# Kernel optimization log

Hardware: AMD Instinct MI355X
Metric: run time of the kernel (lower is better)

## Reference

```python
import jax, jax.numpy as jnp
import numpy as np

NUM_HEADS = 12

def setup_inputs() -> dict:
    key = jax.random.key(0)
    k1, k2, k3 = jax.random.split(key, 3)
    B, H, W, C = 8, 32, 32, 768
    x = jax.random.normal(k1, (B, H, W, C), dtype=jnp.float32)
    qkv_w = jax.random.normal(k2, (3 * C, C), dtype=jnp.float32) * (C ** -0.5)
    qkv_b = jnp.zeros((3 * C,), dtype=jnp.float32)
    proj_w = jax.random.normal(k3, (C, C), dtype=jnp.float32) * (C ** -0.5)
    proj_b = jnp.zeros((C,), dtype=jnp.float32)
    return {"x": x, "qkv_w": qkv_w, "qkv_b": qkv_b, "proj_w": proj_w, "proj_b": proj_b}

def reference(x, qkv_w, qkv_b, proj_w, proj_b):
    B, H, W, C = x.shape
    N = H * W
    h = NUM_HEADS
    d = C // h
    scale = d ** -0.5
    xf = x.reshape(B, N, C)
    # fused QKV projection: [B,N,3C] -> [3,B,h,N,d]
    qkv = (xf @ qkv_w.T + qkv_b).reshape(B, N, 3, h, d).transpose(2, 0, 3, 1, 4)
    q, k, v = qkv[0], qkv[1], qkv[2]  # rope = Identity
    # scaled dot-product attention
    scores = jnp.einsum('bhnd,bhmd->bhnm', q, k) * scale
    attn = jax.nn.softmax(scores, axis=-1)
    out = jnp.einsum('bhnm,bhmd->bhnd', attn, v)
    out = out.transpose(0, 2, 1, 3).reshape(B, N, C)
    out = out @ proj_w.T + proj_b
    return out.reshape(B, H, W, C)
```

## Files before the change

### kernel.cpp

```cpp
#include <hip/hip_runtime.h>
#include <math.h>

#define AS1 __attribute__((address_space(1)))
#define AS3 __attribute__((address_space(3)))

typedef __attribute__((ext_vector_type(8))) short bf16x8;
typedef __attribute__((ext_vector_type(4))) float f32x4;

__device__ __forceinline__ unsigned short f2bf(float f) {
    union { float f; unsigned int i; } v; v.f = f;
    unsigned int r = v.i + 0x7FFFu + ((v.i >> 16) & 1u);
    return (unsigned short)(r >> 16);
}

__device__ __forceinline__ void store_out(float* p, float v) { *p = v; }
__device__ __forceinline__ void store_out(unsigned short* p, float v) { *p = f2bf(v); }

#define N1C (8192 * 768 / 4)
#define N2C (2304 * 768 / 4)
#define N3C (768 * 768 / 4)

__global__ void cvt_all(const float* __restrict__ x, const float* __restrict__ w1,
                        const float* __restrict__ w2,
                        unsigned short* __restrict__ xb, unsigned short* __restrict__ w1b,
                        unsigned short* __restrict__ w2b)
{
    int i = blockIdx.x * blockDim.x + threadIdx.x;
    const float4* s; ushort4* d; int k;
    if (i < N1C)            { s = (const float4*)x;  d = (ushort4*)xb;  k = i; }
    else if (i < N1C + N2C) { s = (const float4*)w1; d = (ushort4*)w1b; k = i - N1C; }
    else if (i < N1C + N2C + N3C) { s = (const float4*)w2; d = (ushort4*)w2b; k = i - N1C - N2C; }
    else return;
    const float4 v = s[k];
    ushort4 o;
    o.x = f2bf(v.x); o.y = f2bf(v.y); o.z = f2bf(v.z); o.w = f2bf(v.w);
    d[k] = o;
}

template <typename OutT>
__global__ __launch_bounds__(256, 2)
void gemm_bt_128(const unsigned short* __restrict__ A,
                 const unsigned short* __restrict__ W,
                 const float* __restrict__ bias,
                 OutT* __restrict__ Cmat,
                 int M, int N, int K)
{
    __shared__ __align__(16) unsigned short As[128 * 32];
    __shared__ __align__(16) unsigned short Bs[128 * 32];

    const int tid  = threadIdx.x;
    const int wave = tid >> 6;
    const int lane = tid & 63;
    const int quad = lane >> 4;
    const int l15  = lane & 15;
    const int wr   = wave >> 1;
    const int wc   = wave & 1;

    const int m0 = blockIdx.x * 128;
    const int n0 = blockIdx.y * 128;

    const int srow = wave * 32 + (lane >> 2);
    const int scol = (lane & 3) * 8;

    const unsigned short* Ag0 = A + (size_t)(m0 + srow) * K + scol;
    const unsigned short* Ag1 = A + (size_t)(m0 + srow + 16) * K + scol;
    const unsigned short* Wg0 = W + (size_t)(n0 + srow) * K + scol;
    const unsigned short* Wg1 = W + (size_t)(n0 + srow + 16) * K + scol;

    unsigned short* As0 = As + (wave * 2 + 0) * 512 + lane * 8;
    unsigned short* As1 = As + (wave * 2 + 1) * 512 + lane * 8;
    unsigned short* Bs0 = Bs + (wave * 2 + 0) * 512 + lane * 8;
    unsigned short* Bs1 = Bs + (wave * 2 + 1) * 512 + lane * 8;

    f32x4 acc[4][4];
#pragma unroll
    for (int i = 0; i < 4; ++i)
#pragma unroll
        for (int j = 0; j < 4; ++j) acc[i][j] = (f32x4){0.f, 0.f, 0.f, 0.f};

    for (int k0 = 0; k0 < K; k0 += 32) {
        __syncthreads();
        __builtin_amdgcn_global_load_lds((AS1 void*)(Ag0 + k0), (AS3 void*)As0, 16, 0, 0);
        __builtin_amdgcn_global_load_lds((AS1 void*)(Ag1 + k0), (AS3 void*)As1, 16, 0, 0);
        __builtin_amdgcn_global_load_lds((AS1 void*)(Wg0 + k0), (AS3 void*)Bs0, 16, 0, 0);
        __builtin_amdgcn_global_load_lds((AS1 void*)(Wg1 + k0), (AS3 void*)Bs1, 16, 0, 0);
        __syncthreads();

        bf16x8 af[4], bfr[4];
#pragma unroll
        for (int i = 0; i < 4; ++i)
            af[i] = *(const bf16x8*)(As + (wr * 64 + i * 16 + l15) * 32 + quad * 8);
#pragma unroll
        for (int j = 0; j < 4; ++j)
            bfr[j] = *(const bf16x8*)(Bs + (wc * 64 + j * 16 + l15) * 32 + quad * 8);
#pragma unroll
        for (int i = 0; i < 4; ++i)
#pragma unroll
            for (int j = 0; j < 4; ++j)
                acc[i][j] = __builtin_amdgcn_mfma_f32_16x16x32_bf16(af[i], bfr[j], acc[i][j], 0, 0, 0);
    }

#pragma unroll
    for (int i = 0; i < 4; ++i) {
        const int row = m0 + wr * 64 + i * 16 + quad * 4;
#pragma unroll
        for (int j = 0; j < 4; ++j) {
            const int col = n0 + wc * 64 + j * 16 + l15;
            const float bv = bias[col];
#pragma unroll
            for (int r = 0; r < 4; ++r)
                store_out(&Cmat[(size_t)(row + r) * N + col], acc[i][j][r] + bv);
        }
    }
}

#define NTOK 1024
#define CCH  768
#define HD   64

__global__ __launch_bounds__(256)
void pack_vT(const unsigned short* __restrict__ qkv, unsigned short* __restrict__ vT)
{
    __shared__ __align__(16) unsigned short Ls[64 * 72];
    const int tile = blockIdx.x;
    const int bh   = blockIdx.y;
    const int b = bh / 12, h = bh % 12;
    const int t = threadIdx.x;

    const int tok = t >> 2, c = (t & 3) * 16;
    const unsigned short* src = qkv + (size_t)(b * NTOK + tile * 64 + tok) * (3 * CCH)
                                    + 2 * CCH + h * HD + c;
    bf16x8 a0 = *(const bf16x8*)src;
    bf16x8 a1 = *(const bf16x8*)(src + 8);
    *(bf16x8*)&Ls[tok * 72 + c]     = a0;
    *(bf16x8*)&Ls[tok * 72 + c + 8] = a1;
    __syncthreads();

    const int r = t >> 5;
    const int dbase = (r >> 1) * 16;
    const int k5b   = (r & 1) * 32;
    unsigned short outv[16];
#pragma unroll
    for (int u = 0; u < 2; ++u) {
        const int L  = (t & 31) * 2 + u;
        const int d  = dbase + (L & 15);
        const int k0 = k5b + (L >> 4) * 8;
#pragma unroll
        for (int j = 0; j < 8; ++j) outv[u * 8 + j] = Ls[(k0 + j) * 72 + d];
    }
    unsigned short* dst = vT + ((size_t)(bh * 16 + tile) * 8 + r) * 512 + (t & 31) * 16;
    *(bf16x8*)dst       = *(bf16x8*)&outv[0];
    *(bf16x8*)(dst + 8) = *(bf16x8*)&outv[8];
}

__global__ __launch_bounds__(256, 3)
void attn_fused(const unsigned short* __restrict__ qkv,
                const unsigned short* __restrict__ vT,
                unsigned short* __restrict__ aout)
{
    __shared__ __align__(16) unsigned short Kf[2][8 * 512];
    __shared__ __align__(16) unsigned short Vt[2][8 * 512];
    __shared__ __align__(16) unsigned short Ps[16 * 512];

    const int tid  = threadIdx.x;
    const int wave = tid >> 6;
    const int lane = tid & 63;
    const int quad = lane >> 4;
    const int l15  = lane & 15;

    const int lin = blockIdx.x;
    const int bh  = lin % 96;
    const int qt  = lin / 96;
    const int b   = bh / 12;
    const int h   = bh % 12;

    const size_t rs = 3 * CCH;
    const unsigned short* Qg = qkv + (size_t)b * NTOK * rs + (size_t)h * HD;
    const unsigned short* Kg = Qg + CCH;
    const unsigned short* vTb = vT + (size_t)bh * 16 * 8 * 512;

    const int q0 = qt * 128;

    bf16x8 qf[2][2];
#pragma unroll
    for (int qb = 0; qb < 2; ++qb)
#pragma unroll
        for (int ks = 0; ks < 2; ++ks)
            qf[qb][ks] = *(const bf16x8*)(Qg + (size_t)(q0 + wave * 32 + qb * 16 + l15) * rs
                                              + ks * 32 + quad * 8);

    f32x4 oacc[2][4];
#pragma unroll
    for (int qb = 0; qb < 2; ++qb)
#pragma unroll
        for (int nb = 0; nb < 4; ++nb) oacc[qb][nb] = (f32x4){0.f, 0.f, 0.f, 0.f};
    float lrow[2] = {0.f, 0.f};

    const unsigned short* kdma = Kg + (size_t)(wave * 16 + l15) * rs + quad * 8;

#pragma unroll
    for (int ks = 0; ks < 2; ++ks)
        __builtin_amdgcn_global_load_lds((AS1 void*)(kdma + ks * 32),
            (AS3 void*)(Kf[0] + (wave * 2 + ks) * 512 + lane * 8), 16, 0, 0);
#pragma unroll
    for (int u = 0; u < 2; ++u)
        __builtin_amdgcn_global_load_lds((AS1 void*)(vTb + (size_t)(wave * 2 + u) * 512 + lane * 8),
            (AS3 void*)(Vt[0] + (wave * 2 + u) * 512 + lane * 8), 16, 0, 0);

    for (int t = 0; t < 16; ++t) {
        const int cur = t & 1;
        __syncthreads();

        if (t < 15) {
            const int nxt = cur ^ 1;
#pragma unroll
            for (int ks = 0; ks < 2; ++ks)
                __builtin_amdgcn_global_load_lds((AS1 void*)(kdma + (size_t)((t + 1) * 64) * rs + ks * 32),
                    (AS3 void*)(Kf[nxt] + (wave * 2 + ks) * 512 + lane * 8), 16, 0, 0);
#pragma unroll
            for (int u = 0; u < 2; ++u)
                __builtin_amdgcn_global_load_lds((AS1 void*)(vTb + ((size_t)(t + 1) * 8 + wave * 2 + u) * 512 + lane * 8),
                    (AS3 void*)(Vt[nxt] + (wave * 2 + u) * 512 + lane * 8), 16, 0, 0);
        }

        f32x4 sacc[2][4];
#pragma unroll
        for (int qb = 0; qb < 2; ++qb)
#pragma unroll
            for (int jk = 0; jk < 4; ++jk) sacc[qb][jk] = (f32x4){0.f, 0.f, 0.f, 0.f};
#pragma unroll
        for (int ks = 0; ks < 2; ++ks) {
            bf16x8 kf[4];
#pragma unroll
            for (int jk = 0; jk < 4; ++jk)
                kf[jk] = *(const bf16x8*)(Kf[cur] + (jk * 2 + ks) * 512 + lane * 8);
#pragma unroll
            for (int qb = 0; qb < 2; ++qb)
#pragma unroll
                for (int jk = 0; jk < 4; ++jk)
                    sacc[qb][jk] = __builtin_amdgcn_mfma_f32_16x16x32_bf16(
                        kf[jk], qf[qb][ks], sacc[qb][jk], 0, 0, 0);
        }

#pragma unroll
        for (int qb = 0; qb < 2; ++qb) {
            float rsum = 0.f;
#pragma unroll
            for (int jk = 0; jk < 4; ++jk)
#pragma unroll
                for (int r = 0; r < 4; ++r) {
                    const float p = __expf(sacc[qb][jk][r] * 0.125f);
                    sacc[qb][jk][r] = p;
                    rsum += p;
                }
            rsum += __shfl_xor(rsum, 16);
            rsum += __shfl_xor(rsum, 32);
            lrow[qb] += rsum;

#pragma unroll
            for (int jk = 0; jk < 4; ++jk) {
                ushort4 pk;
                pk.x = f2bf(sacc[qb][jk][0]);
                pk.y = f2bf(sacc[qb][jk][1]);
                pk.z = f2bf(sacc[qb][jk][2]);
                pk.w = f2bf(sacc[qb][jk][3]);
                const int region = (wave * 2 + qb) * 2 + (jk >> 1);
                const int quadR  = (jk & 1) * 2 + (quad >> 1);
                const int off    = region * 512 + (quadR * 16 + l15) * 8 + (quad & 1) * 4;
                *(ushort4*)&Ps[off] = pk;
            }
        }

#pragma unroll
        for (int ks2 = 0; ks2 < 2; ++ks2) {
            bf16x8 pf[2], vf[4];
#pragma unroll
            for (int qb = 0; qb < 2; ++qb)
                pf[qb] = *(const bf16x8*)(Ps + ((wave * 2 + qb) * 2 + ks2) * 512 + lane * 8);
#pragma unroll
            for (int nb = 0; nb < 4; ++nb)
                vf[nb] = *(const bf16x8*)(Vt[cur] + (nb * 2 + ks2) * 512 + lane * 8);
#pragma unroll
            for (int qb = 0; qb < 2; ++qb)
#pragma unroll
                for (int nb = 0; nb < 4; ++nb)
                    oacc[qb][nb] = __builtin_amdgcn_mfma_f32_16x16x32_bf16(
                        vf[nb], pf[qb], oacc[qb][nb], 0, 0, 0);
        }
    }

#pragma unroll
    for (int qb = 0; qb < 2; ++qb) {
        const float inv = 1.f / lrow[qb];
        const size_t tok = (size_t)(b * NTOK + q0 + wave * 32 + qb * 16 + l15);
#pragma unroll
        for (int nb = 0; nb < 4; ++nb) {
            ushort4 o;
            o.x = f2bf(oacc[qb][nb][0] * inv);
            o.y = f2bf(oacc[qb][nb][1] * inv);
            o.z = f2bf(oacc[qb][nb][2] * inv);
            o.w = f2bf(oacc[qb][nb][3] * inv);
            *(ushort4*)(aout + tok * CCH + h * HD + nb * 16 + quad * 4) = o;
        }
    }
}

extern "C" void kernel_launch(void* const* d_in, const int* in_sizes, int n_in,
                              void* d_out, int out_size, void* d_ws, size_t ws_size,
                              hipStream_t stream)
{
    const float* x      = (const float*)d_in[0];
    const float* qkv_w  = (const float*)d_in[1];
    const float* qkv_b  = (const float*)d_in[2];
    const float* proj_w = (const float*)d_in[3];
    const float* proj_b = (const float*)d_in[4];
    float* out = (float*)d_out;

    unsigned short* qkv = (unsigned short*)d_ws;
    unsigned short* att = qkv + (size_t)8192 * 2304;
    unsigned short* xb  = att + (size_t)8192 * 768;
    unsigned short* wqb = xb  + (size_t)8192 * 768;
    unsigned short* wpb = wqb + (size_t)2304 * 768;
    unsigned short* vT  = xb;

    dim3 blk(256);
    cvt_all<<<dim3((N1C + N2C + N3C + 255) / 256), blk, 0, stream>>>(x, qkv_w, proj_w, xb, wqb, wpb);
    gemm_bt_128<unsigned short><<<dim3(64, 18), blk, 0, stream>>>(xb, wqb, qkv_b, qkv, 8192, 2304, 768);
    pack_vT<<<dim3(16, 96), blk, 0, stream>>>(qkv, vT);
    attn_fused<<<dim3(768), blk, 0, stream>>>(qkv, vT, att);
    gemm_bt_128<float><<<dim3(64, 6), blk, 0, stream>>>(att, wpb, proj_b, out, 8192, 768, 768);
}
```

Before: 207.0 us.

## Fuse V transpose into QKV GEMM epilogue and fold softmax scale into Q

The QKV GEMM now gets its own kernel whose epilogue writes Q and K into a narrower 1536-wide buffer, with Q pre-scaled by 1/sqrt(d), and writes V directly in the transposed tiled layout the attention kernel expects. This removes the separate pack_vT kernel and its extra read and write of V. The attention kernel halves its P staging buffer by interleaving P stores with PV MFMAs per k-half, raises launch bounds occupancy to 4, and uses a cheaper perm-based bf16 packing. The new packing rounds with a plain +0x8000 instead of round-to-nearest-even, which slightly changes numerics.

Result: faster. 187.0 us (-9.7%).

```diff
diff --git a/kernel.cpp b/kernel.cpp
--- a/kernel.cpp
+++ b/kernel.cpp
@@ -13,8 +13,18 @@
     return (unsigned short)(r >> 16);
 }
 
+__device__ __forceinline__ unsigned int pack2bf(float lo, float hi) {
+    union { float f; unsigned int i; } a, b; a.f = lo; b.f = hi;
+    return __builtin_amdgcn_perm(b.i + 0x8000u, a.i + 0x8000u, 0x07060302u);
+}
+
 __device__ __forceinline__ void store_out(float* p, float v) { *p = v; }
 __device__ __forceinline__ void store_out(unsigned short* p, float v) { *p = f2bf(v); }
+
+#define NTOK 1024
+#define CCH  768
+#define HD   64
+#define QKS  1536
 
 #define N1C (8192 * 768 / 4)
 #define N2C (2304 * 768 / 4)
@@ -114,53 +124,118 @@
     }
 }
 
-#define NTOK 1024
-#define CCH  768
-#define HD   64
-
-__global__ __launch_bounds__(256)
-void pack_vT(const unsigned short* __restrict__ qkv, unsigned short* __restrict__ vT)
+__global__ __launch_bounds__(256, 2)
+void gemm_qkv(const unsigned short* __restrict__ A,
+              const unsigned short* __restrict__ W,
+              const float* __restrict__ bias,
+              unsigned short* __restrict__ qk,
+              unsigned short* __restrict__ vT)
 {
-    __shared__ __align__(16) unsigned short Ls[64 * 72];
-    const int tile = blockIdx.x;
-    const int bh   = blockIdx.y;
-    const int b = bh / 12, h = bh % 12;
-    const int t = threadIdx.x;
-
-    const int tok = t >> 2, c = (t & 3) * 16;
-    const unsigned short* src = qkv + (size_t)(b * NTOK + tile * 64 + tok) * (3 * CCH)
-                                    + 2 * CCH + h * HD + c;
-    bf16x8 a0 = *(const bf16x8*)src;
-    bf16x8 a1 = *(const bf16x8*)(src + 8);
-    *(bf16x8*)&Ls[tok * 72 + c]     = a0;
-    *(bf16x8*)&Ls[tok * 72 + c + 8] = a1;
-    __syncthreads();
-
-    const int r = t >> 5;
-    const int dbase = (r >> 1) * 16;
-    const int k5b   = (r & 1) * 32;
-    unsigned short outv[16];
-#pragma unroll
-    for (int u = 0; u < 2; ++u) {
-        const int L  = (t & 31) * 2 + u;
-        const int d  = dbase + (L & 15);
-        const int k0 = k5b + (L >> 4) * 8;
-#pragma unroll
-        for (int j = 0; j < 8; ++j) outv[u * 8 + j] = Ls[(k0 + j) * 72 + d];
-    }
-    unsigned short* dst = vT + ((size_t)(bh * 16 + tile) * 8 + r) * 512 + (t & 31) * 16;
-    *(bf16x8*)dst       = *(bf16x8*)&outv[0];
-    *(bf16x8*)(dst + 8) = *(bf16x8*)&outv[8];
-}
-
-__global__ __launch_bounds__(256, 3)
-void attn_fused(const unsigned short* __restrict__ qkv,
+    const int N = 2304, K = 768;
+    __shared__ __align__(16) unsigned short As[128 * 32];
+    __shared__ __align__(16) unsigned short Bs[128 * 32];
+
+    const int tid  = threadIdx.x;
+    const int wave = tid >> 6;
+    const int lane = tid & 63;
+    const int quad = lane >> 4;
+    const int l15  = lane & 15;
+    const int wr   = wave >> 1;
+    const int wc   = wave & 1;
+
+    const int m0 = blockIdx.x * 128;
+    const int n0 = blockIdx.y * 128;
+
+    const int srow = wave * 32 + (lane >> 2);
+    const int scol = (lane & 3) * 8;
+
+    const unsigned short* Ag0 = A + (size_t)(m0 + srow) * K + scol;
+    const unsigned short* Ag1 = A + (size_t)(m0 + srow + 16) * K + scol;
+    const unsigned short* Wg0 = W + (size_t)(n0 + srow) * K + scol;
+    const unsigned short* Wg1 = W + (size_t)(n0 + srow + 16) * K + scol;
+
+    unsigned short* As0 = As + (wave * 2 + 0) * 512 + lane * 8;
+    unsigned short* As1 = As + (wave * 2 + 1) * 512 + lane * 8;
+    unsigned short* Bs0 = Bs + (wave * 2 + 0) * 512 + lane * 8;
+    unsigned short* Bs1 = Bs + (wave * 2 + 1) * 512 + lane * 8;
+
+    f32x4 acc[4][4];
+#pragma unroll
+    for (int i = 0; i < 4; ++i)
+#pragma unroll
+        for (int j = 0; j < 4; ++j) acc[i][j] = (f32x4){0.f, 0.f, 0.f, 0.f};
+
+    for (int k0 = 0; k0 < K; k0 += 32) {
+        __syncthreads();
+        __builtin_amdgcn_global_load_lds((AS1 void*)(Ag0 + k0), (AS3 void*)As0, 16, 0, 0);
+        __builtin_amdgcn_global_load_lds((AS1 void*)(Ag1 + k0), (AS3 void*)As1, 16, 0, 0);
+        __builtin_amdgcn_global_load_lds((AS1 void*)(Wg0 + k0), (AS3 void*)Bs0, 16, 0, 0);
+        __builtin_amdgcn_global_load_lds((AS1 void*)(Wg1 + k0), (AS3 void*)Bs1, 16, 0, 0);
+        __syncthreads();
+
+        bf16x8 af[4], bfr[4];
+#pragma unroll
+        for (int i = 0; i < 4; ++i)
+            af[i] = *(const bf16x8*)(As + (wr * 64 + i * 16 + l15) * 32 + quad * 8);
+#pragma unroll
+        for (int j = 0; j < 4; ++j)
+            bfr[j] = *(const bf16x8*)(Bs + (wc * 64 + j * 16 + l15) * 32 + quad * 8);
+#pragma unroll
+        for (int i = 0; i < 4; ++i)
+#pragma unroll
+            for (int j = 0; j < 4; ++j)
+                acc[i][j] = __builtin_amdgcn_mfma_f32_16x16x32_bf16(af[i], bfr[j], acc[i][j], 0, 0, 0);
+    }
+
+    const int colbase = n0 + wc * 64;
+    if (colbase < 1536) {
+        const float s = (colbase < 768) ? 0.125f : 1.f;
+#pragma unroll
+        for (int i = 0; i < 4; ++i) {
+            const int row = m0 + wr * 64 + i * 16 + quad * 4;
+#pragma unroll
+            for (int j = 0; j < 4; ++j) {
+                const int col = colbase + j * 16 + l15;
+                const float bv = bias[col];
+#pragma unroll
+                for (int r = 0; r < 4; ++r)
+                    qk[(size_t)(row + r) * QKS + col] = f2bf((acc[i][j][r] + bv) * s);
+            }
+        }
+    } else {
+#pragma unroll
+        for (int i = 0; i < 4; ++i) {
+            const int m    = m0 + wr * 64 + i * 16 + quad * 4;
+            const int b    = m >> 10;
+            const int tok  = m & 1023;
+            const int tile = tok >> 6;
+            const int K0   = tok & 63;
+#pragma unroll
+            for (int j = 0; j < 4; ++j) {
+                const int col = colbase + j * 16 + l15;
+                const int c   = col - 1536;
+                const int h   = c >> 6, d = c & 63;
+                const float bv = bias[col];
+                const int bh     = b * 12 + h;
+                const int region = (d >> 4) * 2 + (K0 >> 5);
+                const int L      = ((K0 >> 3) & 3) * 16 + (d & 15);
+                uint2 o;
+                o.x = pack2bf(acc[i][j][0] + bv, acc[i][j][1] + bv);
+                o.y = pack2bf(acc[i][j][2] + bv, acc[i][j][3] + bv);
+                *(uint2*)(vT + (((size_t)(bh * 16 + tile) * 8 + region) << 9) + L * 8 + (K0 & 7)) = o;
+            }
+        }
+    }
+}
+
+__global__ __launch_bounds__(256, 4)
+void attn_fused(const unsigned short* __restrict__ qk,
                 const unsigned short* __restrict__ vT,
                 unsigned short* __restrict__ aout)
 {
     __shared__ __align__(16) unsigned short Kf[2][8 * 512];
     __shared__ __align__(16) unsigned short Vt[2][8 * 512];
-    __shared__ __align__(16) unsigned short Ps[16 * 512];
+    __shared__ __align__(16) unsigned short Ps[8 * 512];
 
     const int tid  = threadIdx.x;
     const int wave = tid >> 6;
@@ -174,9 +249,8 @@
     const int b   = bh / 12;
     const int h   = bh % 12;
 
-    const size_t rs = 3 * CCH;
-    const unsigned short* Qg = qkv + (size_t)b * NTOK * rs + (size_t)h * HD;
-    const unsigned short* Kg = Qg + CCH;
+    const unsigned short* Qg  = qk + (size_t)b * NTOK * QKS + (size_t)h * HD;
+    const unsigned short* Kg  = Qg + CCH;
     const unsigned short* vTb = vT + (size_t)bh * 16 * 8 * 512;
 
     const int q0 = qt * 128;
@@ -186,7 +260,7 @@
     for (int qb = 0; qb < 2; ++qb)
 #pragma unroll
         for (int ks = 0; ks < 2; ++ks)
-            qf[qb][ks] = *(const bf16x8*)(Qg + (size_t)(q0 + wave * 32 + qb * 16 + l15) * rs
+            qf[qb][ks] = *(const bf16x8*)(Qg + (size_t)(q0 + wave * 32 + qb * 16 + l15) * QKS
                                               + ks * 32 + quad * 8);
 
     f32x4 oacc[2][4];
@@ -196,7 +270,7 @@
         for (int nb = 0; nb < 4; ++nb) oacc[qb][nb] = (f32x4){0.f, 0.f, 0.f, 0.f};
     float lrow[2] = {0.f, 0.f};
 
-    const unsigned short* kdma = Kg + (size_t)(wave * 16 + l15) * rs + quad * 8;
+    const unsigned short* kdma = Kg + (size_t)(wave * 16 + l15) * QKS + quad * 8;
 
 #pragma unroll
     for (int ks = 0; ks < 2; ++ks)
@@ -215,7 +289,7 @@
             const int nxt = cur ^ 1;
 #pragma unroll
             for (int ks = 0; ks < 2; ++ks)
-                __builtin_amdgcn_global_load_lds((AS1 void*)(kdma + (size_t)((t + 1) * 64) * rs + ks * 32),
+                __builtin_amdgcn_global_load_lds((AS1 void*)(kdma + (size_t)((t + 1) * 64) * QKS + ks * 32),
                     (AS3 void*)(Kf[nxt] + (wave * 2 + ks) * 512 + lane * 8), 16, 0, 0);
 #pragma unroll
             for (int u = 0; u < 2; ++u)
@@ -249,37 +323,36 @@
             for (int jk = 0; jk < 4; ++jk)
 #pragma unroll
                 for (int r = 0; r < 4; ++r) {
-                    const float p = __expf(sacc[qb][jk][r] * 0.125f);
+                    const float p = __expf(sacc[qb][jk][r]);
                     sacc[qb][jk][r] = p;
                     rsum += p;
                 }
             rsum += __shfl_xor(rsum, 16);
             rsum += __shfl_xor(rsum, 32);
             lrow[qb] += rsum;
-
-#pragma unroll
-            for (int jk = 0; jk < 4; ++jk) {
-                ushort4 pk;
-                pk.x = f2bf(sacc[qb][jk][0]);
-                pk.y = f2bf(sacc[qb][jk][1]);
-                pk.z = f2bf(sacc[qb][jk][2]);
-                pk.w = f2bf(sacc[qb][jk][3]);
-                const int region = (wave * 2 + qb) * 2 + (jk >> 1);
-                const int quadR  = (jk & 1) * 2 + (quad >> 1);
-                const int off    = region * 512 + (quadR * 16 + l15) * 8 + (quad & 1) * 4;
-                *(ushort4*)&Ps[off] = pk;
-            }
-        }
-
-#pragma unroll
-        for (int ks2 = 0; ks2 < 2; ++ks2) {
+        }
+
+#pragma unroll
+        for (int p = 0; p < 2; ++p) {
+#pragma unroll
+            for (int qb = 0; qb < 2; ++qb)
+#pragma unroll
+                for (int jh = 0; jh < 2; ++jh) {
+                    const int jk = 2 * p + jh;
+                    uint2 o;
+                    o.x = pack2bf(sacc[qb][jk][0], sacc[qb][jk][1]);
+                    o.y = pack2bf(sacc[qb][jk][2], sacc[qb][jk][3]);
+                    const int off = (wave * 2 + qb) * 512
+                                  + ((jh * 2 + (quad >> 1)) * 16 + l15) * 8 + (quad & 1) * 4;
+                    *(uint2*)&Ps[off] = o;
+                }
             bf16x8 pf[2], vf[4];
 #pragma unroll
             for (int qb = 0; qb < 2; ++qb)
-                pf[qb] = *(const bf16x8*)(Ps + ((wave * 2 + qb) * 2 + ks2) * 512 + lane * 8);
+                pf[qb] = *(const bf16x8*)(Ps + (wave * 2 + qb) * 512 + lane * 8);
 #pragma unroll
             for (int nb = 0; nb < 4; ++nb)
-                vf[nb] = *(const bf16x8*)(Vt[cur] + (nb * 2 + ks2) * 512 + lane * 8);
+                vf[nb] = *(const bf16x8*)(Vt[cur] + (nb * 2 + p) * 512 + lane * 8);
 #pragma unroll
             for (int qb = 0; qb < 2; ++qb)
 #pragma unroll
@@ -295,12 +368,10 @@
         const size_t tok = (size_t)(b * NTOK + q0 + wave * 32 + qb * 16 + l15);
 #pragma unroll
         for (int nb = 0; nb < 4; ++nb) {
-            ushort4 o;
-            o.x = f2bf(oacc[qb][nb][0] * inv);
-            o.y = f2bf(oacc[qb][nb][1] * inv);
-            o.z = f2bf(oacc[qb][nb][2] * inv);
-            o.w = f2bf(oacc[qb][nb][3] * inv);
-            *(ushort4*)(aout + tok * CCH + h * HD + nb * 16 + quad * 4) = o;
+            uint2 o;
+            o.x = pack2bf(oacc[qb][nb][0] * inv, oacc[qb][nb][1] * inv);
+            o.y = pack2bf(oacc[qb][nb][2] * inv, oacc[qb][nb][3] * inv);
+            *(uint2*)(aout + tok * CCH + h * HD + nb * 16 + quad * 4) = o;
         }
     }
 }
@@ -316,17 +387,16 @@
     const float* proj_b = (const float*)d_in[4];
     float* out = (float*)d_out;
 
-    unsigned short* qkv = (unsigned short*)d_ws;
-    unsigned short* att = qkv + (size_t)8192 * 2304;
+    unsigned short* qk  = (unsigned short*)d_ws;
+    unsigned short* att = qk  + (size_t)8192 * 1536;
     unsigned short* xb  = att + (size_t)8192 * 768;
     unsigned short* wqb = xb  + (size_t)8192 * 768;
     unsigned short* wpb = wqb + (size_t)2304 * 768;
-    unsigned short* vT  = xb;
+    unsigned short* vT  = wpb + (size_t)768 * 768;
 
     dim3 blk(256);
     cvt_all<<<dim3((N1C + N2C + N3C + 255) / 256), blk, 0, stream>>>(x, qkv_w, proj_w, xb, wqb, wpb);
-    gemm_bt_128<unsigned short><<<dim3(64, 18), blk, 0, stream>>>(xb, wqb, qkv_b, qkv, 8192, 2304, 768);
-    pack_vT<<<dim3(16, 96), blk, 0, stream>>>(qkv, vT);
-    attn_fused<<<dim3(768), blk, 0, stream>>>(qkv, vT, att);
+    gemm_qkv<<<dim3(64, 18), blk, 0, stream>>>(xb, wqb, qkv_b, qk, vT);
+    attn_fused<<<dim3(768), blk, 0, stream>>>(qk, vT, att);
     gemm_bt_128<float><<<dim3(64, 6), blk, 0, stream>>>(att, wpb, proj_b, out, 8192, 768, 768);
 }
```
